# Performance work log

Measured on AMD Instinct MI355X. Metric: run time of the kernel, lower is better.

Reference implementation:

```python
import jax, jax.numpy as jnp
import numpy as np

HEADS, DIM_HEAD = 8, 64
EPS = 1e-5  # torch InstanceNorm1d default


def instance_norm(t):
    # torch InstanceNorm1d(dim_head) applied to (b*h, n, d) normalizes over the
    # last dim d for each (b, h, n); affine=False, biased variance.
    mu = jnp.mean(t, axis=-1, keepdims=True)
    var = jnp.mean((t - mu) ** 2, axis=-1, keepdims=True)
    return (t - mu) * jax.lax.rsqrt(var + EPS)


def setup_inputs() -> dict:
    key = jax.random.key(0)
    k1, k2, k3, k4 = jax.random.split(key, 4)
    B, N, D = 8, 8192, 256
    inner = HEADS * DIM_HEAD  # 512
    x = jax.random.normal(k1, (B, N, D), jnp.float32)
    w_qkv = jax.random.normal(k2, (3 * inner, D), jnp.float32) / np.sqrt(D).astype(np.float32)
    w_out = jax.random.normal(k3, (D, inner), jnp.float32) / np.sqrt(inner).astype(np.float32)
    b_out = 0.01 * jax.random.normal(k4, (D,), jnp.float32)
    return {"x": x, "w_qkv": w_qkv, "w_out": w_out, "b_out": b_out}


def reference(x, w_qkv, w_out, b_out):
    B, N, _ = x.shape
    H, Dh = HEADS, DIM_HEAD
    # fused qkv projection: [B,N,3*H*Dh]
    qkv = jnp.einsum('bnd,ed->bne', x, w_qkv)
    q, k, v = jnp.split(qkv, 3, axis=-1)

    def to_heads(t):
        return t.reshape(B, N, H, Dh).transpose(0, 2, 1, 3)  # b h n d

    q, k, v = to_heads(q), to_heads(k), to_heads(v)
    # galerkin: instance-norm K and V
    k = instance_norm(k)
    v = instance_norm(v)
    # linear (non-softmax) attention: (K^T V) then Q @ (K^T V), scaled by 1/N
    dots = jnp.einsum('bhnd,bhne->bhde', k, v)            # [B,H,Dh,Dh]
    out = jnp.einsum('bhnd,bhde->bhne', q, dots) / N      # [B,H,N,Dh]
    out = out.transpose(0, 2, 1, 3).reshape(B, N, H * Dh)
    return jnp.einsum('bne,de->bnd', out, w_out) + b_out
```

## Files before the change

### kernel.cpp

```cpp
#include <hip/hip_runtime.h>
#include <hip/hip_bf16.h>
#include <stdint.h>

typedef __attribute__((ext_vector_type(8))) __bf16 bf16x8;
typedef __attribute__((ext_vector_type(8))) unsigned short ushort8_t;
typedef __attribute__((ext_vector_type(4))) unsigned short ushort4_t;
typedef __attribute__((ext_vector_type(4))) float f32x4;

#define MFMA16(a, b, c) __builtin_amdgcn_mfma_f32_16x16x32_bf16((a), (b), (c), 0, 0, 0)

static __device__ __forceinline__ unsigned short f2bf(float f) {
  union { float f; unsigned u; } v; v.f = f;
  unsigned r = v.u + 0x7fffu + ((v.u >> 16) & 1u);
  return (unsigned short)(r >> 16);
}
static __device__ __forceinline__ float bf2f(unsigned short u) {
  union { unsigned u; float f; } v; v.u = ((unsigned)u) << 16; return v.f;
}

static __device__ __forceinline__ void gld_lds16(const void* g, void* l) {
  __builtin_amdgcn_global_load_lds((const __attribute__((address_space(1))) void*)g,
                                   (__attribute__((address_space(3))) void*)l, 16, 0, 0);
}

__global__ __launch_bounds__(256) void k_convx(const float* __restrict__ x,
                                               unsigned short* __restrict__ xb) {
  size_t i = ((size_t)blockIdx.x * 256 + threadIdx.x) * 4;
  float4 v = *(const float4*)(x + i);
  ushort4_t o = { f2bf(v.x), f2bf(v.y), f2bf(v.z), f2bf(v.w) };
  *(ushort4_t*)(xb + i) = o;
}

__global__ void k_convw(const float* __restrict__ w, unsigned short* __restrict__ wb) {
  int i = (blockIdx.x * 256 + threadIdx.x) * 4;
  float4 v = *(const float4*)(w + i);
  ushort4_t o = { f2bf(v.x), f2bf(v.y), f2bf(v.z), f2bf(v.w) };
  *(ushort4_t*)(wb + i) = o;
}

__global__ void k_convo(const float* __restrict__ w, unsigned short* __restrict__ wb) {
  int i = (blockIdx.x * 256 + threadIdx.x) * 4;
  float4 v = *(const float4*)(w + i);
  ushort4_t o = { f2bf(v.x), f2bf(v.y), f2bf(v.z), f2bf(v.w) };
  *(ushort4_t*)(wb + i) = o;
}

__global__ __launch_bounds__(512) void k_fused(const unsigned short* __restrict__ xb,
                                               const unsigned short* __restrict__ wqb,
                                               float* __restrict__ partials) {
  __shared__ __align__(16) char smem[65536];
  unsigned short* As = (unsigned short*)smem;
  unsigned short* Bs = (unsigned short*)(smem + 32768);
  unsigned short* kt = (unsigned short*)smem;
  unsigned short* vt = (unsigned short*)(smem + 18432);

  const int t = threadIdx.x;
  const int w = t >> 6, lane = t & 63, lr = lane & 15, lg = lane >> 4;
  const int wr = w >> 1, wc = w & 1;
  const int dblk = w >> 1, ep = w & 1;

  const int id = blockIdx.x;
  const int nid = (id & 7) * 128 + (id >> 3);
  const int mg = nid >> 3, h = nid & 7;

  const int srl = lane >> 3, sc = lane & 7;
  const int swz = (sc ^ srl) << 3;

  const unsigned short* bptr[2];
  int aoff[2];
#pragma unroll
  for (int i = 0; i < 2; ++i) {
    const int br = (w * 2 + i) * 8 + srl;
    const int grow = (br < 64) ? (512 + h * 64 + br) : (1024 + h * 64 + (br - 64));
    bptr[i] = wqb + (size_t)grow * 256 + swz;
    aoff[i] = br * 256 + swz;
  }

  f32x4 acc2[2] = {f32x4{0.f, 0.f, 0.f, 0.f}, f32x4{0.f, 0.f, 0.f, 0.f}};

  for (int mi = 0; mi < 4; ++mi) {
    const long m0 = ((long)mg * 4 + mi) * 128;
    const unsigned short* am = xb + (size_t)m0 * 256;

#pragma unroll
    for (int i = 0; i < 2; ++i) {
      gld_lds16(am + aoff[i], &As[(w * 2 + i) * 512]);
      gld_lds16(bptr[i],      &Bs[(w * 2 + i) * 512]);
    }
    __syncthreads();

    f32x4 acc[2][4];
#pragma unroll
    for (int mb = 0; mb < 2; ++mb)
#pragma unroll
      for (int nb = 0; nb < 4; ++nb) acc[mb][nb] = f32x4{0.f, 0.f, 0.f, 0.f};

    for (int ktt = 0; ktt < 4; ++ktt) {
      const int cur = ktt & 1, nxt = cur ^ 1;
      if (ktt < 3) {
        const int k0 = (ktt + 1) * 64;
#pragma unroll
        for (int i = 0; i < 2; ++i) {
          gld_lds16(am + aoff[i] + k0, &As[nxt * 8192 + (w * 2 + i) * 512]);
          gld_lds16(bptr[i] + k0,      &Bs[nxt * 8192 + (w * 2 + i) * 512]);
        }
      }
      bf16x8 a[2][2], b[4][2];
#pragma unroll
      for (int mb = 0; mb < 2; ++mb) {
        const int R = wr * 32 + mb * 16 + lr;
#pragma unroll
        for (int kh = 0; kh < 2; ++kh)
          a[mb][kh] = *(const bf16x8*)&As[cur * 8192 + R * 64 + ((((kh << 2) + lg) ^ (R & 7)) << 3)];
      }
#pragma unroll
      for (int nb = 0; nb < 4; ++nb) {
        const int E = wc * 64 + nb * 16 + lr;
#pragma unroll
        for (int kh = 0; kh < 2; ++kh)
          b[nb][kh] = *(const bf16x8*)&Bs[cur * 8192 + E * 64 + ((((kh << 2) + lg) ^ (E & 7)) << 3)];
      }
#pragma unroll
      for (int mb = 0; mb < 2; ++mb)
#pragma unroll
        for (int nb = 0; nb < 4; ++nb)
#pragma unroll
          for (int kh = 0; kh < 2; ++kh)
            acc[mb][nb] = MFMA16(a[mb][kh], b[nb][kh], acc[mb][nb]);
      __syncthreads();
    }

    unsigned short* dst = (wc == 0) ? kt : vt;
#pragma unroll
    for (int mb = 0; mb < 2; ++mb) {
#pragma unroll
      for (int rg = 0; rg < 4; ++rg) {
        float s1 = acc[mb][0][rg] + acc[mb][1][rg] + acc[mb][2][rg] + acc[mb][3][rg];
        float s2 = acc[mb][0][rg] * acc[mb][0][rg] + acc[mb][1][rg] * acc[mb][1][rg] +
                   acc[mb][2][rg] * acc[mb][2][rg] + acc[mb][3][rg] * acc[mb][3][rg];
        s1 += __shfl_xor(s1, 1); s2 += __shfl_xor(s2, 1);
        s1 += __shfl_xor(s1, 2); s2 += __shfl_xor(s2, 2);
        s1 += __shfl_xor(s1, 4); s2 += __shfl_xor(s2, 4);
        s1 += __shfl_xor(s1, 8); s2 += __shfl_xor(s2, 8);
        const float mean = s1 * (1.f / 64.f);
        const float rs = rsqrtf(s2 * (1.f / 64.f) - mean * mean + 1e-5f);
        const int n = wr * 32 + mb * 16 + lg * 4 + rg;
        const int cn = n >> 6, nn = n & 63;
#pragma unroll
        for (int nb = 0; nb < 4; ++nb)
          dst[cn * 4608 + (nb * 16 + lr) * 72 + nn] = f2bf((acc[mb][nb][rg] - mean) * rs);
      }
    }
    __syncthreads();

#pragma unroll
    for (int cn = 0; cn < 2; ++cn) {
#pragma unroll
      for (int ns = 0; ns < 64; ns += 32) {
        bf16x8 af = *(const bf16x8*)&kt[cn * 4608 + (dblk * 16 + lr) * 72 + ns + lg * 8];
#pragma unroll
        for (int e = 0; e < 2; ++e) {
          bf16x8 bv = *(const bf16x8*)&vt[cn * 4608 + ((ep * 2 + e) * 16 + lr) * 72 + ns + lg * 8];
          acc2[e] = MFMA16(af, bv, acc2[e]);
        }
      }
    }
    __syncthreads();
  }

  float* pb = partials + ((size_t)mg * 8 + h) * 4096;
#pragma unroll
  for (int e = 0; e < 2; ++e)
#pragma unroll
    for (int rg = 0; rg < 4; ++rg) {
      const int d = dblk * 16 + lg * 4 + rg;
      const int eo = (ep * 2 + e) * 16 + lr;
      pb[d * 64 + eo] = acc2[e][rg];
    }
}

__global__ __launch_bounds__(256) void k_mmat(const float* __restrict__ partials,
                                              const float* __restrict__ wqkv,
                                              unsigned short* __restrict__ tmpT) {
  __shared__ float dl[4096];
  __shared__ float wqls[64 * 256];
  const int bh = blockIdx.x, b = bh >> 3, h = bh & 7;
  const int t = threadIdx.x;
#pragma unroll
  for (int i = 0; i < 4; ++i) {
    int off = t * 16 + i * 4;
    f32x4 s = {0.f, 0.f, 0.f, 0.f};
    for (int c = 0; c < 16; ++c) {
      const size_t chunk = (size_t)(b * 16 + c) * 8 + h;
      f32x4 p = *(const f32x4*)(partials + chunk * 4096 + off);
      s += p;
    }
    *(f32x4*)&dl[off] = s;
  }
#pragma unroll
  for (int i = 0; i < 16; ++i) {
    int idx4 = i * 256 + t;
    int d = idx4 >> 6, c4 = idx4 & 63;
    *(f32x4*)&wqls[d * 256 + c4 * 4] =
        *(const f32x4*)(wqkv + (size_t)(h * 64 + d) * 256 + c4 * 4);
  }
  __syncthreads();
  const int k = t;
  const float scale = 1.0f / 8192.0f;
  float res[64];
  for (int e = 0; e < 64; ++e) {
    float s = 0.f;
#pragma unroll
    for (int d = 0; d < 64; ++d) s += dl[d * 64 + e] * wqls[d * 256 + k];
    res[e] = s * scale;
  }
  unsigned short* dstp = tmpT + (size_t)b * 131072 + (size_t)k * 512 + h * 64;
#pragma unroll
  for (int e8 = 0; e8 < 8; ++e8) {
    ushort8_t o;
#pragma unroll
    for (int j = 0; j < 8; ++j) o[j] = f2bf(res[e8 * 8 + j]);
    *(ushort8_t*)(dstp + e8 * 8) = o;
  }
}

__global__ __launch_bounds__(256) void k_pmat(const unsigned short* __restrict__ woutb,
                                              const unsigned short* __restrict__ tmpT,
                                              unsigned short* __restrict__ pswz) {
  const int bid = blockIdx.x;
  const int b = bid >> 2, oq = (bid >> 1) & 1, kq = bid & 1;
  const int t = threadIdx.x, w = t >> 6, lane = t & 63, lr = lane & 15, lg = lane >> 4;
  const int wr = w >> 1, wc = w & 1;
  const int ob = oq * 128 + wr * 64, kb = kq * 128 + wc * 64;
  const unsigned short* tb = tmpT + (size_t)b * 131072;

  f32x4 acc[4][4];
#pragma unroll
  for (int mb = 0; mb < 4; ++mb)
#pragma unroll
    for (int nb = 0; nb < 4; ++nb) acc[mb][nb] = f32x4{0.f, 0.f, 0.f, 0.f};

  for (int ks = 0; ks < 16; ++ks) {
    bf16x8 a[4], bb[4];
#pragma unroll
    for (int mb = 0; mb < 4; ++mb)
      a[mb] = *(const bf16x8*)(woutb + (size_t)(ob + mb * 16 + lr) * 512 + ks * 32 + lg * 8);
#pragma unroll
    for (int nb = 0; nb < 4; ++nb)
      bb[nb] = *(const bf16x8*)(tb + (size_t)(kb + nb * 16 + lr) * 512 + ks * 32 + lg * 8);
#pragma unroll
    for (int mb = 0; mb < 4; ++mb)
#pragma unroll
      for (int nb = 0; nb < 4; ++nb) acc[mb][nb] = MFMA16(a[mb], bb[nb], acc[mb][nb]);
  }

  unsigned short* pb = pswz + (size_t)b * 65536;
#pragma unroll
  for (int mb = 0; mb < 4; ++mb)
#pragma unroll
    for (int nb = 0; nb < 4; ++nb)
#pragma unroll
      for (int rg = 0; rg < 4; ++rg) {
        int o = ob + mb * 16 + lg * 4 + rg;
        int k = kb + nb * 16 + lr;
        pb[(((k >> 5) * 16 + (o >> 4)) * 64 + (o & 15) + ((k >> 3) & 3) * 16) * 8 + (k & 7)] =
            f2bf(acc[mb][nb][rg]);
      }
}

__global__ __launch_bounds__(512) void k_gemm2(const unsigned short* __restrict__ xb,
                                               const unsigned short* __restrict__ pswz,
                                               const float* __restrict__ bout,
                                               float* __restrict__ out) {
  __shared__ unsigned short As[2][128 * 64];
  const int b = blockIdx.x >> 6, mt = blockIdx.x & 63;
  const long m0 = (long)mt * 128;
  const int t = threadIdx.x, w = t >> 6, lane = t & 63, lr = lane & 15, lg = lane >> 4;
  const int wr = w >> 2, wc = w & 3;
  const unsigned short* qb = xb + ((size_t)b * 8192 + m0) * 256;
  const unsigned short* Mb = pswz + (size_t)b * 65536;
  const int srl = lane >> 3, sc = lane & 7;

#pragma unroll
  for (int i = 0; i < 2; ++i) {
    const int row = (i * 8 + w) * 8 + srl;
    gld_lds16(qb + (size_t)row * 256 + ((sc ^ (row & 7)) << 3),
              &As[0][(i * 8 + w) * 512]);
  }
  __syncthreads();

  f32x4 acc[4][4];
#pragma unroll
  for (int mb = 0; mb < 4; ++mb)
#pragma unroll
    for (int nb = 0; nb < 4; ++nb) acc[mb][nb] = f32x4{0.f, 0.f, 0.f, 0.f};

  for (int ks = 0; ks < 4; ++ks) {
    const int cur = ks & 1, nxt = cur ^ 1;
    if (ks < 3) {
      const int k0 = (ks + 1) * 64;
#pragma unroll
      for (int i = 0; i < 2; ++i) {
        const int row = (i * 8 + w) * 8 + srl;
        gld_lds16(qb + (size_t)row * 256 + k0 + ((sc ^ (row & 7)) << 3),
                  &As[nxt][(i * 8 + w) * 512]);
      }
    }
    bf16x8 a[4][2], bfr[2][4];
#pragma unroll
    for (int mb = 0; mb < 4; ++mb) {
      const int R = wr * 64 + mb * 16 + lr;
#pragma unroll
      for (int kh = 0; kh < 2; ++kh)
        a[mb][kh] = *(const bf16x8*)&As[cur][R * 64 + ((((kh << 2) + lg) ^ (R & 7)) << 3)];
    }
#pragma unroll
    for (int kh = 0; kh < 2; ++kh)
#pragma unroll
      for (int nb = 0; nb < 4; ++nb)
        bfr[kh][nb] = *(const bf16x8*)(Mb + ((((size_t)ks * 2 + kh) * 16 + wc * 4 + nb) * 64 + lane) * 8);
#pragma unroll
    for (int mb = 0; mb < 4; ++mb)
#pragma unroll
      for (int nb = 0; nb < 4; ++nb)
#pragma unroll
        for (int kh = 0; kh < 2; ++kh)
          acc[mb][nb] = MFMA16(a[mb][kh], bfr[kh][nb], acc[mb][nb]);
    __syncthreads();
  }

  float bo[4];
#pragma unroll
  for (int nb = 0; nb < 4; ++nb) bo[nb] = bout[wc * 64 + nb * 16 + lr];
  float* ob = out + ((size_t)b * 8192 + m0) * 256;
#pragma unroll
  for (int mb = 0; mb < 4; ++mb)
#pragma unroll
    for (int nb = 0; nb < 4; ++nb)
#pragma unroll
      for (int rg = 0; rg < 4; ++rg) {
        int row = wr * 64 + mb * 16 + lg * 4 + rg;
        int c = wc * 64 + nb * 16 + lr;
        ob[(size_t)row * 256 + c] = acc[mb][nb][rg] + bo[nb];
      }
}

extern "C" void kernel_launch(void* const* d_in, const int* in_sizes, int n_in,
                              void* d_out, int out_size, void* d_ws, size_t ws_size,
                              hipStream_t stream) {
  const float* x    = (const float*)d_in[0];
  const float* wqkv = (const float*)d_in[1];
  const float* wout = (const float*)d_in[2];
  const float* bout = (const float*)d_in[3];
  float* out = (float*)d_out;

  char* ws = (char*)d_ws;
  unsigned short* xb = (unsigned short*)ws;
  size_t off = (size_t)65536 * 256 * 2;
  unsigned short* wqb = (unsigned short*)(ws + off);
  off += (size_t)1536 * 256 * 2;
  unsigned short* woutb = (unsigned short*)(ws + off);
  off += (size_t)256 * 512 * 2;
  float* partials = (float*)(ws + off);
  off += (size_t)1024 * 4096 * 4;
  unsigned short* tmpT = (unsigned short*)(ws + off);
  off += (size_t)8 * 131072 * 2;
  unsigned short* pswz = (unsigned short*)(ws + off);
  off += (size_t)8 * 65536 * 2;

  k_convx<<<16384, 256, 0, stream>>>(x, xb);
  k_convw<<<384, 256, 0, stream>>>(wqkv, wqb);
  k_convo<<<128, 256, 0, stream>>>(wout, woutb);
  k_fused<<<1024, 512, 0, stream>>>(xb, wqb, partials);
  k_mmat<<<64, 256, 0, stream>>>(partials, wqkv, tmpT);
  k_pmat<<<32, 256, 0, stream>>>(woutb, tmpT, pswz);
  k_gemm2<<<512, 512, 0, stream>>>(xb, pswz, bout, out);
}
```

Measured before the change: 166.0 us.

## Merge conversion kernels and prefetch next A tile during K^T V stage

The three fp32-to-bf16 conversion kernels become one grid-stride kernel, cutting launch overhead. In the fused projection kernel the normalized K/V staging moves to the B-buffer half of shared memory and uses an XOR swizzle instead of padded rows. This frees the A buffer, so the next m-tile's A load is issued before the K^T V MFMA stage and the B reload right after it, hiding load latency across iterations. The risk is added ordering complexity around shared-memory overlap, and the grid-stride conversion may achieve lower bandwidth than the one-element-per-thread kernels.

After: 173.7 us. 4.6% more time.

```diff
diff --git a/kernel.cpp b/kernel.cpp
--- a/kernel.cpp
+++ b/kernel.cpp
@@ -23,26 +23,25 @@
                                    (__attribute__((address_space(3))) void*)l, 16, 0, 0);
 }
 
-__global__ __launch_bounds__(256) void k_convx(const float* __restrict__ x,
-                                               unsigned short* __restrict__ xb) {
-  size_t i = ((size_t)blockIdx.x * 256 + threadIdx.x) * 4;
-  float4 v = *(const float4*)(x + i);
-  ushort4_t o = { f2bf(v.x), f2bf(v.y), f2bf(v.z), f2bf(v.w) };
-  *(ushort4_t*)(xb + i) = o;
-}
-
-__global__ void k_convw(const float* __restrict__ w, unsigned short* __restrict__ wb) {
-  int i = (blockIdx.x * 256 + threadIdx.x) * 4;
-  float4 v = *(const float4*)(w + i);
-  ushort4_t o = { f2bf(v.x), f2bf(v.y), f2bf(v.z), f2bf(v.w) };
-  *(ushort4_t*)(wb + i) = o;
-}
-
-__global__ void k_convo(const float* __restrict__ w, unsigned short* __restrict__ wb) {
-  int i = (blockIdx.x * 256 + threadIdx.x) * 4;
-  float4 v = *(const float4*)(w + i);
-  ushort4_t o = { f2bf(v.x), f2bf(v.y), f2bf(v.z), f2bf(v.w) };
-  *(ushort4_t*)(wb + i) = o;
+__global__ __launch_bounds__(256) void k_conv(const float* __restrict__ x,
+                                              const float* __restrict__ wqkv,
+                                              const float* __restrict__ wout,
+                                              unsigned short* __restrict__ xb,
+                                              unsigned short* __restrict__ wqb,
+                                              unsigned short* __restrict__ woutb) {
+  const size_t NX = 4194304;
+  const size_t NW = 98304;
+  const size_t NO = 32768;
+  const size_t stride = (size_t)gridDim.x * 256;
+  for (size_t i4 = (size_t)blockIdx.x * 256 + threadIdx.x; i4 < NX + NW + NO; i4 += stride) {
+    const float* src; unsigned short* dst; size_t off;
+    if (i4 < NX)           { src = x;    dst = xb;    off = i4; }
+    else if (i4 < NX + NW) { src = wqkv; dst = wqb;   off = i4 - NX; }
+    else                   { src = wout; dst = woutb; off = i4 - NX - NW; }
+    float4 v = ((const float4*)src)[off];
+    ushort4_t o = { f2bf(v.x), f2bf(v.y), f2bf(v.z), f2bf(v.w) };
+    *(ushort4_t*)(dst + off * 4) = o;
+  }
 }
 
 __global__ __launch_bounds__(512) void k_fused(const unsigned short* __restrict__ xb,
@@ -51,8 +50,7 @@
   __shared__ __align__(16) char smem[65536];
   unsigned short* As = (unsigned short*)smem;
   unsigned short* Bs = (unsigned short*)(smem + 32768);
-  unsigned short* kt = (unsigned short*)smem;
-  unsigned short* vt = (unsigned short*)(smem + 18432);
+  unsigned short* ovl = (unsigned short*)(smem + 32768);
 
   const int t = threadIdx.x;
   const int w = t >> 6, lane = t & 63, lr = lane & 15, lg = lane >> 4;
@@ -78,15 +76,17 @@
 
   f32x4 acc2[2] = {f32x4{0.f, 0.f, 0.f, 0.f}, f32x4{0.f, 0.f, 0.f, 0.f}};
 
+  {
+    const unsigned short* am0 = xb + ((size_t)mg * 4 * 128) * 256;
+#pragma unroll
+    for (int i = 0; i < 2; ++i) {
+      gld_lds16(am0 + aoff[i], &As[(w * 2 + i) * 512]);
+      gld_lds16(bptr[i],       &Bs[(w * 2 + i) * 512]);
+    }
+  }
+
   for (int mi = 0; mi < 4; ++mi) {
-    const long m0 = ((long)mg * 4 + mi) * 128;
-    const unsigned short* am = xb + (size_t)m0 * 256;
-
-#pragma unroll
-    for (int i = 0; i < 2; ++i) {
-      gld_lds16(am + aoff[i], &As[(w * 2 + i) * 512]);
-      gld_lds16(bptr[i],      &Bs[(w * 2 + i) * 512]);
-    }
+    const unsigned short* am = xb + ((size_t)(mg * 4 + mi) * 128) * 256;
     __syncthreads();
 
     f32x4 acc[2][4];
@@ -130,7 +130,7 @@
       __syncthreads();
     }
 
-    unsigned short* dst = (wc == 0) ? kt : vt;
+    unsigned short* dst = ovl + wc * 8192;
 #pragma unroll
     for (int mb = 0; mb < 2; ++mb) {
 #pragma unroll
@@ -146,26 +146,46 @@
         const float rs = rsqrtf(s2 * (1.f / 64.f) - mean * mean + 1e-5f);
         const int n = wr * 32 + mb * 16 + lg * 4 + rg;
         const int cn = n >> 6, nn = n & 63;
-#pragma unroll
-        for (int nb = 0; nb < 4; ++nb)
-          dst[cn * 4608 + (nb * 16 + lr) * 72 + nn] = f2bf((acc[mb][nb][rg] - mean) * rs);
+        const int cc = nn >> 3, cj = nn & 7;
+#pragma unroll
+        for (int nb = 0; nb < 4; ++nb) {
+          const int d = nb * 16 + lr;
+          dst[cn * 4096 + d * 64 + ((cc ^ (d & 7)) << 3) + cj] =
+              f2bf((acc[mb][nb][rg] - mean) * rs);
+        }
       }
     }
     __syncthreads();
 
+    if (mi < 3) {
+      const unsigned short* amn = am + 128 * 256;
+#pragma unroll
+      for (int i = 0; i < 2; ++i)
+        gld_lds16(amn + aoff[i], &As[(w * 2 + i) * 512]);
+    }
+
 #pragma unroll
     for (int cn = 0; cn < 2; ++cn) {
 #pragma unroll
       for (int ns = 0; ns < 64; ns += 32) {
-        bf16x8 af = *(const bf16x8*)&kt[cn * 4608 + (dblk * 16 + lr) * 72 + ns + lg * 8];
+        const int cA = (ns >> 3) + lg;
+        const int dd = dblk * 16 + lr;
+        bf16x8 af = *(const bf16x8*)&ovl[cn * 4096 + dd * 64 + ((cA ^ (dd & 7)) << 3)];
 #pragma unroll
         for (int e = 0; e < 2; ++e) {
-          bf16x8 bv = *(const bf16x8*)&vt[cn * 4608 + ((ep * 2 + e) * 16 + lr) * 72 + ns + lg * 8];
+          const int ee = (ep * 2 + e) * 16 + lr;
+          bf16x8 bv = *(const bf16x8*)&ovl[8192 + cn * 4096 + ee * 64 + ((cA ^ (ee & 7)) << 3)];
           acc2[e] = MFMA16(af, bv, acc2[e]);
         }
       }
     }
     __syncthreads();
+
+    if (mi < 3) {
+#pragma unroll
+      for (int i = 0; i < 2; ++i)
+        gld_lds16(bptr[i], &Bs[(w * 2 + i) * 512]);
+    }
   }
 
   float* pb = partials + ((size_t)mg * 8 + h) * 4096;
@@ -368,9 +388,7 @@
   unsigned short* pswz = (unsigned short*)(ws + off);
   off += (size_t)8 * 65536 * 2;
 
-  k_convx<<<16384, 256, 0, stream>>>(x, xb);
-  k_convw<<<384, 256, 0, stream>>>(wqkv, wqb);
-  k_convo<<<128, 256, 0, stream>>>(wout, woutb);
+  k_conv<<<4096, 256, 0, stream>>>(x, wqkv, wout, xb, wqb, woutb);
   k_fused<<<1024, 512, 0, stream>>>(xb, wqb, partials);
   k_mmat<<<64, 256, 0, stream>>>(partials, wqkv, tmpT);
   k_pmat<<<32, 256, 0, stream>>>(woutb, tmpT, pswz);
```
